# Kernel optimization log

Measured on AMD Instinct MI355X. Metric: run time of the kernel, lower is better.

The kernel has to match this reference:

```python
import jax, jax.numpy as jnp
import numpy as np

BS, V, N, C_IN, C_OUT = 8, 4096, 16, 64, 64


def setup_inputs() -> dict:
    key = jax.random.key(0)
    k1, k2, k3, k4, k5 = jax.random.split(key, 5)
    stdv = 1.0 / np.sqrt(N * C_IN)
    return {
        "neighbor_index": jax.random.randint(k1, (BS, V, N), 0, V, dtype=jnp.int64),
        "vertices": jax.random.normal(k2, (BS, V, 3), dtype=jnp.float32),
        "feature_map": jax.random.normal(k3, (BS, V, C_IN), dtype=jnp.float32),
        "weights": jax.random.uniform(k4, (C_OUT, (N + 1) * C_IN), dtype=jnp.float32, minval=-stdv, maxval=stdv),
        "bias": jax.random.uniform(k5, (C_OUT,), dtype=jnp.float32, minval=-stdv, maxval=stdv),
    }


def reference(neighbor_index, vertices, feature_map, weights, bias):
    bs, v, n = neighbor_index.shape
    # gather neighbor features per batch element: (bs, v, n, c)
    neighbors = jax.vmap(lambda f, idx: f[idx])(feature_map, neighbor_index)
    # prepend self feature: (bs, v, n+1, c)
    feats = jnp.concatenate([feature_map[:, :, None, :], neighbors], axis=2)
    # torch permutes to (bs, c, n+1, v) then reshapes -> flat index = c*(n+1)+k,
    # equivalent to transposing last two dims here before flattening
    flat = feats.transpose(0, 1, 3, 2).reshape(bs, v, -1)  # (bs, v, c*(n+1))
    out = jnp.einsum('bvf,of->bvo', flat, weights) + bias
    return jax.nn.relu(out)
```

## Files before the change

kernel.cpp:

```cpp
#include <hip/hip_runtime.h>
#include <stdint.h>

#define NV 4096

typedef __attribute__((ext_vector_type(8))) short bf16x8;
typedef __attribute__((ext_vector_type(4))) float f32x4;

__device__ __forceinline__ unsigned short f2bf(float f) {
  union { float f; unsigned int u; } v; v.f = f;
  unsigned int r = v.u + 0x7FFF + ((v.u >> 16) & 1);
  return (unsigned short)(r >> 16);
}

__global__ __launch_bounds__(256)
void prep(const float* __restrict__ fm, const float* __restrict__ w,
          unsigned short* __restrict__ fmb, unsigned short* __restrict__ wb) {
  int blk = blockIdx.x;
  if (blk < 1024) {
    int i = (blk * 256 + threadIdx.x) * 8;
    float4 v0 = *(const float4*)(fm + i);
    float4 v1 = *(const float4*)(fm + i + 4);
    ushort4 o0, o1;
    o0.x = f2bf(v0.x); o0.y = f2bf(v0.y); o0.z = f2bf(v0.z); o0.w = f2bf(v0.w);
    o1.x = f2bf(v1.x); o1.y = f2bf(v1.y); o1.z = f2bf(v1.z); o1.w = f2bf(v1.w);
    *(ushort4*)(fmb + i) = o0;
    *(ushort4*)(fmb + i + 4) = o1;
  } else {
    int t = (blk - 1024) * 256 + threadIdx.x;
    int c = t & 63;
    int o = (t >> 6) & 63;
    int k = t >> 12;
    wb[t] = f2bf(w[o * 1088 + c * 17 + k]);
  }
}

__global__ __launch_bounds__(512, 2)
void conv_main(const int* __restrict__ nbr, const unsigned short* __restrict__ fmb,
               const unsigned short* __restrict__ wb, const float* __restrict__ bias,
               float* __restrict__ out) {
  __shared__ unsigned short smem[17 * 4096];

  const int bid = blockIdx.x;
  const int b = bid & 7;
  const int tile = bid >> 3;
  const int tid = threadIdx.x;
  const int lane = tid & 63;
  const int lm = lane & 15;
  const int lk = lane >> 4;
  const int w8 = tid >> 6;
  const int rg = w8 >> 1;
  const int h = w8 & 1;

  const int rbase = tile * 128 + rg * 32;
  const int row0 = rbase + lm;
  const int row1 = rbase + 16 + lm;

  const bf16x8* fb = (const bf16x8*)(fmb + (size_t)b * NV * 64);

  const int4* n0 = (const int4*)(nbr + ((size_t)b * NV + row0) * 16) + h * 2;
  const int4* n1 = (const int4*)(nbr + ((size_t)b * NV + row1) * 16) + h * 2;
  const int4 i0a = n0[0], i0b = n0[1];
  const int4 i1a = n1[0], i1b = n1[1];

  const int off0 = lm * 128 + ((lk ^ (lm & 7)) << 4);
  const int off1 = off0 ^ 64;

  f32x4 acc00{0,0,0,0}, acc01{0,0,0,0}, acc02{0,0,0,0}, acc03{0,0,0,0};
  f32x4 acc10{0,0,0,0}, acc11{0,0,0,0}, acc12{0,0,0,0}, acc13{0,0,0,0};

  bf16x8 A0h0X, A0h1X, A1h0X, A1h1X;
  bf16x8 A0h0Y, A0h1Y, A1h0Y, A1h1Y;
  bf16x8 A0h0Z, A0h1Z, A1h0Z, A1h1Z;
  bf16x8 B0h0P, B1h0P, B2h0P, B3h0P, B0h1P, B1h1P, B2h1P, B3h1P;
  bf16x8 B0h0Q, B1h0Q, B2h0Q, B3h0Q, B0h1Q, B1h1Q, B2h1Q, B3h1Q;

#define SBR __builtin_amdgcn_sched_barrier(0)
#define MFMA __builtin_amdgcn_mfma_f32_16x16x32_bf16

#define LOADA(S, SV0, SV1) {                         \
    const bf16x8* p0_ = fb + (size_t)(SV0) * 8;      \
    const bf16x8* p1_ = fb + (size_t)(SV1) * 8;      \
    A0h0##S = p0_[lk];     A0h1##S = p0_[lk + 4];    \
    A1h0##S = p1_[lk];     A1h1##S = p1_[lk + 4];    \
  }

#define LOADB(S, KG) {                                          \
    const char* bp_ = ((const char*)smem) + (KG) * 8192;        \
    B0h0##S = *(const bf16x8*)(bp_ + 0 * 2048 + off0);          \
    B1h0##S = *(const bf16x8*)(bp_ + 1 * 2048 + off0);          \
    B2h0##S = *(const bf16x8*)(bp_ + 2 * 2048 + off0);          \
    B3h0##S = *(const bf16x8*)(bp_ + 3 * 2048 + off0);          \
    B0h1##S = *(const bf16x8*)(bp_ + 0 * 2048 + off1);          \
    B1h1##S = *(const bf16x8*)(bp_ + 1 * 2048 + off1);          \
    B2h1##S = *(const bf16x8*)(bp_ + 2 * 2048 + off1);          \
    B3h1##S = *(const bf16x8*)(bp_ + 3 * 2048 + off1);          \
  }

#define MM(SA, SB) {                                       \
    acc00 = MFMA(A0h0##SA, B0h0##SB, acc00, 0, 0, 0);      \
    acc01 = MFMA(A0h0##SA, B1h0##SB, acc01, 0, 0, 0);      \
    acc02 = MFMA(A0h0##SA, B2h0##SB, acc02, 0, 0, 0);      \
    acc03 = MFMA(A0h0##SA, B3h0##SB, acc03, 0, 0, 0);      \
    acc10 = MFMA(A1h0##SA, B0h0##SB, acc10, 0, 0, 0);      \
    acc11 = MFMA(A1h0##SA, B1h0##SB, acc11, 0, 0, 0);      \
    acc12 = MFMA(A1h0##SA, B2h0##SB, acc12, 0, 0, 0);      \
    acc13 = MFMA(A1h0##SA, B3h0##SB, acc13, 0, 0, 0);      \
    acc00 = MFMA(A0h1##SA, B0h1##SB, acc00, 0, 0, 0);      \
    acc01 = MFMA(A0h1##SA, B1h1##SB, acc01, 0, 0, 0);      \
    acc02 = MFMA(A0h1##SA, B2h1##SB, acc02, 0, 0, 0);      \
    acc03 = MFMA(A0h1##SA, B3h1##SB, acc03, 0, 0, 0);      \
    acc10 = MFMA(A1h1##SA, B0h1##SB, acc10, 0, 0, 0);      \
    acc11 = MFMA(A1h1##SA, B1h1##SB, acc11, 0, 0, 0);      \
    acc12 = MFMA(A1h1##SA, B2h1##SB, acc12, 0, 0, 0);      \
    acc13 = MFMA(A1h1##SA, B3h1##SB, acc13, 0, 0, 0);      \
  }

  const int sv00 = h ? i0a.x : row0;   const int sv10 = h ? i1a.x : row1;
  const int sv01 = h ? i0a.y : i0a.x;  const int sv11 = h ? i1a.y : i1a.x;
  const int sv02 = h ? i0a.z : i0a.y;  const int sv12 = h ? i1a.z : i1a.y;

  LOADA(X, sv00, sv10);
  LOADA(Y, sv01, sv11);

  #pragma unroll
  for (int i = 0; i < 17; ++i) {
    int t = i * 512 + tid;
    int slot = t >> 9;
    int r = (t >> 3) & 63;
    int sl = t & 7;
    int seg = sl ^ (r & 7);
    const unsigned short* src = wb + (size_t)slot * 4096 + r * 64 + seg * 8;
    unsigned short* dst = smem + (size_t)t * 8;
    __builtin_amdgcn_global_load_lds(
        (const __attribute__((address_space(1))) void*)src,
        (__attribute__((address_space(3))) void*)dst, 16, 0, 0);
  }
  __syncthreads();

  LOADA(Z, sv02, sv12);
  if (h == 0) { LOADB(P, 0); } else { LOADB(P, 9); }

  if (h == 0) {
    LOADB(Q, 1); SBR; MM(X, P); SBR; LOADA(X, i0a.z, i1a.z); SBR;
    LOADB(P, 2); SBR; MM(Y, Q); SBR; LOADA(Y, i0a.w, i1a.w); SBR;
    LOADB(Q, 3); SBR; MM(Z, P); SBR; LOADA(Z, i0b.x, i1b.x); SBR;
    LOADB(P, 4); SBR; MM(X, Q); SBR; LOADA(X, i0b.y, i1b.y); SBR;
    LOADB(Q, 5); SBR; MM(Y, P); SBR; LOADA(Y, i0b.z, i1b.z); SBR;
    LOADB(P, 6); SBR; MM(Z, Q); SBR; LOADA(Z, i0b.w, i1b.w); SBR;
    LOADB(Q, 7); SBR; MM(X, P); SBR;
    LOADB(P, 8); SBR; MM(Y, Q); SBR;
    MM(Z, P);
  } else {
    LOADB(Q, 10); SBR; MM(X, P); SBR; LOADA(X, i0a.w, i1a.w); SBR;
    LOADB(P, 11); SBR; MM(Y, Q); SBR; LOADA(Y, i0b.x, i1b.x); SBR;
    LOADB(Q, 12); SBR; MM(Z, P); SBR; LOADA(Z, i0b.y, i1b.y); SBR;
    LOADB(P, 13); SBR; MM(X, Q); SBR; LOADA(X, i0b.z, i1b.z); SBR;
    LOADB(Q, 14); SBR; MM(Y, P); SBR; LOADA(Y, i0b.w, i1b.w); SBR;
    LOADB(P, 15); SBR; MM(Z, Q); SBR;
    LOADB(Q, 16); SBR; MM(X, P); SBR;
    MM(Y, Q);
  }

#undef MM
#undef LOADB
#undef LOADA
#undef MFMA
#undef SBR

  __syncthreads();
  if (h == 1) {
    float* rp = (float*)smem + rg * 2048 + lane * 4;
    *(f32x4*)(rp + 0 * 256) = acc00;
    *(f32x4*)(rp + 1 * 256) = acc01;
    *(f32x4*)(rp + 2 * 256) = acc02;
    *(f32x4*)(rp + 3 * 256) = acc03;
    *(f32x4*)(rp + 4 * 256) = acc10;
    *(f32x4*)(rp + 5 * 256) = acc11;
    *(f32x4*)(rp + 6 * 256) = acc12;
    *(f32x4*)(rp + 7 * 256) = acc13;
  }
  __syncthreads();
  if (h == 0) {
    const float* rp = (const float*)smem + rg * 2048 + lane * 4;
    acc00 += *(const f32x4*)(rp + 0 * 256);
    acc01 += *(const f32x4*)(rp + 1 * 256);
    acc02 += *(const f32x4*)(rp + 2 * 256);
    acc03 += *(const f32x4*)(rp + 3 * 256);
    acc10 += *(const f32x4*)(rp + 4 * 256);
    acc11 += *(const f32x4*)(rp + 5 * 256);
    acc12 += *(const f32x4*)(rp + 6 * 256);
    acc13 += *(const f32x4*)(rp + 7 * 256);

    const float bv0 = bias[lm];
    const float bv1 = bias[16 + lm];
    const float bv2 = bias[32 + lm];
    const float bv3 = bias[48 + lm];
    float* op = out + (size_t)b * NV * 64;
    #pragma unroll
    for (int m = 0; m < 2; ++m) {
      const int gv = rbase + m * 16 + lk * 4;
      #pragma unroll
      for (int r = 0; r < 4; ++r) {
        float* orow = op + (size_t)(gv + r) * 64;
        if (m == 0) {
          orow[lm]      = fmaxf(acc00[r] + bv0, 0.f);
          orow[16 + lm] = fmaxf(acc01[r] + bv1, 0.f);
          orow[32 + lm] = fmaxf(acc02[r] + bv2, 0.f);
          orow[48 + lm] = fmaxf(acc03[r] + bv3, 0.f);
        } else {
          orow[lm]      = fmaxf(acc10[r] + bv0, 0.f);
          orow[16 + lm] = fmaxf(acc11[r] + bv1, 0.f);
          orow[32 + lm] = fmaxf(acc12[r] + bv2, 0.f);
          orow[48 + lm] = fmaxf(acc13[r] + bv3, 0.f);
        }
      }
    }
  }
}

extern "C" void kernel_launch(void* const* d_in, const int* in_sizes, int n_in,
                              void* d_out, int out_size, void* d_ws, size_t ws_size,
                              hipStream_t stream) {
  const int* nbr = (const int*)d_in[0];
  const float* fm = (const float*)d_in[2];
  const float* w = (const float*)d_in[3];
  const float* bias = (const float*)d_in[4];
  float* out = (float*)d_out;

  unsigned short* fmb = (unsigned short*)d_ws;
  unsigned short* wb = fmb + (size_t)8 * NV * 64;

  prep<<<1296, 256, 0, stream>>>(fm, w, fmb, wb);
  conv_main<<<256, 512, 0, stream>>>(nbr, fmb, wb, bias, out);
}
```

Baseline: 22.99 us.

## Issue all neighbor gathers upfront, swap MFMA operands for vectorized output stores

All 9 (or 8) neighbor feature rows per wave are gathered into registers before the weight LDS wait, using a manual vmcnt wait and s_barrier in place of the rolling double-buffered A/B schedule. MFMA operands are swapped (weights as A, features as B), so each lane's accumulator holds four consecutive output channels. This lets the epilogue write float4 stores and load bias as vectors. The aim is more memory-level parallelism for the gathers and fewer scalar global stores, at the cost of much higher VGPR pressure and reliance on a hand-tuned vmcnt count.

```diff
diff --git a/kernel.cpp b/kernel.cpp
--- a/kernel.cpp
+++ b/kernel.cpp
@@ -57,70 +57,10 @@
 
   const bf16x8* fb = (const bf16x8*)(fmb + (size_t)b * NV * 64);
 
-  const int4* n0 = (const int4*)(nbr + ((size_t)b * NV + row0) * 16) + h * 2;
-  const int4* n1 = (const int4*)(nbr + ((size_t)b * NV + row1) * 16) + h * 2;
-  const int4 i0a = n0[0], i0b = n0[1];
-  const int4 i1a = n1[0], i1b = n1[1];
-
-  const int off0 = lm * 128 + ((lk ^ (lm & 7)) << 4);
-  const int off1 = off0 ^ 64;
-
-  f32x4 acc00{0,0,0,0}, acc01{0,0,0,0}, acc02{0,0,0,0}, acc03{0,0,0,0};
-  f32x4 acc10{0,0,0,0}, acc11{0,0,0,0}, acc12{0,0,0,0}, acc13{0,0,0,0};
-
-  bf16x8 A0h0X, A0h1X, A1h0X, A1h1X;
-  bf16x8 A0h0Y, A0h1Y, A1h0Y, A1h1Y;
-  bf16x8 A0h0Z, A0h1Z, A1h0Z, A1h1Z;
-  bf16x8 B0h0P, B1h0P, B2h0P, B3h0P, B0h1P, B1h1P, B2h1P, B3h1P;
-  bf16x8 B0h0Q, B1h0Q, B2h0Q, B3h0Q, B0h1Q, B1h1Q, B2h1Q, B3h1Q;
-
-#define SBR __builtin_amdgcn_sched_barrier(0)
-#define MFMA __builtin_amdgcn_mfma_f32_16x16x32_bf16
-
-#define LOADA(S, SV0, SV1) {                         \
-    const bf16x8* p0_ = fb + (size_t)(SV0) * 8;      \
-    const bf16x8* p1_ = fb + (size_t)(SV1) * 8;      \
-    A0h0##S = p0_[lk];     A0h1##S = p0_[lk + 4];    \
-    A1h0##S = p1_[lk];     A1h1##S = p1_[lk + 4];    \
-  }
-
-#define LOADB(S, KG) {                                          \
-    const char* bp_ = ((const char*)smem) + (KG) * 8192;        \
-    B0h0##S = *(const bf16x8*)(bp_ + 0 * 2048 + off0);          \
-    B1h0##S = *(const bf16x8*)(bp_ + 1 * 2048 + off0);          \
-    B2h0##S = *(const bf16x8*)(bp_ + 2 * 2048 + off0);          \
-    B3h0##S = *(const bf16x8*)(bp_ + 3 * 2048 + off0);          \
-    B0h1##S = *(const bf16x8*)(bp_ + 0 * 2048 + off1);          \
-    B1h1##S = *(const bf16x8*)(bp_ + 1 * 2048 + off1);          \
-    B2h1##S = *(const bf16x8*)(bp_ + 2 * 2048 + off1);          \
-    B3h1##S = *(const bf16x8*)(bp_ + 3 * 2048 + off1);          \
-  }
-
-#define MM(SA, SB) {                                       \
-    acc00 = MFMA(A0h0##SA, B0h0##SB, acc00, 0, 0, 0);      \
-    acc01 = MFMA(A0h0##SA, B1h0##SB, acc01, 0, 0, 0);      \
-    acc02 = MFMA(A0h0##SA, B2h0##SB, acc02, 0, 0, 0);      \
-    acc03 = MFMA(A0h0##SA, B3h0##SB, acc03, 0, 0, 0);      \
-    acc10 = MFMA(A1h0##SA, B0h0##SB, acc10, 0, 0, 0);      \
-    acc11 = MFMA(A1h0##SA, B1h0##SB, acc11, 0, 0, 0);      \
-    acc12 = MFMA(A1h0##SA, B2h0##SB, acc12, 0, 0, 0);      \
-    acc13 = MFMA(A1h0##SA, B3h0##SB, acc13, 0, 0, 0);      \
-    acc00 = MFMA(A0h1##SA, B0h1##SB, acc00, 0, 0, 0);      \
-    acc01 = MFMA(A0h1##SA, B1h1##SB, acc01, 0, 0, 0);      \
-    acc02 = MFMA(A0h1##SA, B2h1##SB, acc02, 0, 0, 0);      \
-    acc03 = MFMA(A0h1##SA, B3h1##SB, acc03, 0, 0, 0);      \
-    acc10 = MFMA(A1h1##SA, B0h1##SB, acc10, 0, 0, 0);      \
-    acc11 = MFMA(A1h1##SA, B1h1##SB, acc11, 0, 0, 0);      \
-    acc12 = MFMA(A1h1##SA, B2h1##SB, acc12, 0, 0, 0);      \
-    acc13 = MFMA(A1h1##SA, B3h1##SB, acc13, 0, 0, 0);      \
-  }
-
-  const int sv00 = h ? i0a.x : row0;   const int sv10 = h ? i1a.x : row1;
-  const int sv01 = h ? i0a.y : i0a.x;  const int sv11 = h ? i1a.y : i1a.x;
-  const int sv02 = h ? i0a.z : i0a.y;  const int sv12 = h ? i1a.z : i1a.y;
-
-  LOADA(X, sv00, sv10);
-  LOADA(Y, sv01, sv11);
+  const int4* q0 = (const int4*)(nbr + ((size_t)b * NV + row0) * 16) + h * 2;
+  const int4* q1 = (const int4*)(nbr + ((size_t)b * NV + row1) * 16) + h * 2;
+  const int4 i0a = q0[0], i0b = q0[1];
+  const int4 i1a = q1[0], i1b = q1[1];
 
   #pragma unroll
   for (int i = 0; i < 17; ++i) {
@@ -135,37 +75,91 @@
         (const __attribute__((address_space(1))) void*)src,
         (__attribute__((address_space(3))) void*)dst, 16, 0, 0);
   }
-  __syncthreads();
-
-  LOADA(Z, sv02, sv12);
-  if (h == 0) { LOADB(P, 0); } else { LOADB(P, 9); }
+  __builtin_amdgcn_sched_barrier(0);
+
+  bf16x8 F0m0h0, F0m0h1, F0m1h0, F0m1h1;
+  bf16x8 F1m0h0, F1m0h1, F1m1h0, F1m1h1;
+  bf16x8 F2m0h0, F2m0h1, F2m1h0, F2m1h1;
+  bf16x8 F3m0h0, F3m0h1, F3m1h0, F3m1h1;
+  bf16x8 F4m0h0, F4m0h1, F4m1h0, F4m1h1;
+  bf16x8 F5m0h0, F5m0h1, F5m1h0, F5m1h1;
+  bf16x8 F6m0h0, F6m0h1, F6m1h0, F6m1h1;
+  bf16x8 F7m0h0, F7m0h1, F7m1h0, F7m1h1;
+  bf16x8 F8m0h0, F8m0h1, F8m1h0, F8m1h1;
+
+#define LOADF(J, SV0, SV1) {                          \
+    const bf16x8* p0_ = fb + (size_t)(SV0) * 8;       \
+    const bf16x8* p1_ = fb + (size_t)(SV1) * 8;       \
+    F##J##m0h0 = p0_[lk];  F##J##m0h1 = p0_[lk + 4];  \
+    F##J##m1h0 = p1_[lk];  F##J##m1h1 = p1_[lk + 4];  \
+  }
 
   if (h == 0) {
-    LOADB(Q, 1); SBR; MM(X, P); SBR; LOADA(X, i0a.z, i1a.z); SBR;
-    LOADB(P, 2); SBR; MM(Y, Q); SBR; LOADA(Y, i0a.w, i1a.w); SBR;
-    LOADB(Q, 3); SBR; MM(Z, P); SBR; LOADA(Z, i0b.x, i1b.x); SBR;
-    LOADB(P, 4); SBR; MM(X, Q); SBR; LOADA(X, i0b.y, i1b.y); SBR;
-    LOADB(Q, 5); SBR; MM(Y, P); SBR; LOADA(Y, i0b.z, i1b.z); SBR;
-    LOADB(P, 6); SBR; MM(Z, Q); SBR; LOADA(Z, i0b.w, i1b.w); SBR;
-    LOADB(Q, 7); SBR; MM(X, P); SBR;
-    LOADB(P, 8); SBR; MM(Y, Q); SBR;
-    MM(Z, P);
+    LOADF(0, row0, row1);
+    LOADF(1, i0a.x, i1a.x); LOADF(2, i0a.y, i1a.y);
+    LOADF(3, i0a.z, i1a.z); LOADF(4, i0a.w, i1a.w);
+    LOADF(5, i0b.x, i1b.x); LOADF(6, i0b.y, i1b.y);
+    LOADF(7, i0b.z, i1b.z); LOADF(8, i0b.w, i1b.w);
   } else {
-    LOADB(Q, 10); SBR; MM(X, P); SBR; LOADA(X, i0a.w, i1a.w); SBR;
-    LOADB(P, 11); SBR; MM(Y, Q); SBR; LOADA(Y, i0b.x, i1b.x); SBR;
-    LOADB(Q, 12); SBR; MM(Z, P); SBR; LOADA(Z, i0b.y, i1b.y); SBR;
-    LOADB(P, 13); SBR; MM(X, Q); SBR; LOADA(X, i0b.z, i1b.z); SBR;
-    LOADB(Q, 14); SBR; MM(Y, P); SBR; LOADA(Y, i0b.w, i1b.w); SBR;
-    LOADB(P, 15); SBR; MM(Z, Q); SBR;
-    LOADB(Q, 16); SBR; MM(X, P); SBR;
-    MM(Y, Q);
-  }
-
-#undef MM
-#undef LOADB
-#undef LOADA
+    LOADF(0, i0a.x, i1a.x); LOADF(1, i0a.y, i1a.y);
+    LOADF(2, i0a.z, i1a.z); LOADF(3, i0a.w, i1a.w);
+    LOADF(4, i0b.x, i1b.x); LOADF(5, i0b.y, i1b.y);
+    LOADF(6, i0b.z, i1b.z); LOADF(7, i0b.w, i1b.w);
+  }
+
+  __builtin_amdgcn_sched_barrier(0);
+  if (h == 0) { asm volatile("s_waitcnt vmcnt(36)" ::: "memory"); }
+  else        { asm volatile("s_waitcnt vmcnt(32)" ::: "memory"); }
+  __builtin_amdgcn_sched_barrier(0);
+  __builtin_amdgcn_s_barrier();
+  __builtin_amdgcn_sched_barrier(0);
+
+  const int off0 = lm * 128 + ((lk ^ (lm & 7)) << 4);
+  const int off1 = off0 ^ 64;
+
+  f32x4 acc00{0,0,0,0}, acc01{0,0,0,0}, acc02{0,0,0,0}, acc03{0,0,0,0};
+  f32x4 acc10{0,0,0,0}, acc11{0,0,0,0}, acc12{0,0,0,0}, acc13{0,0,0,0};
+
+#define MFMA __builtin_amdgcn_mfma_f32_16x16x32_bf16
+#define PHASE(J, SLOT) {                                            \
+    const char* bp_ = ((const char*)smem) + (SLOT) * 8192;          \
+    bf16x8 W0a = *(const bf16x8*)(bp_ + 0 * 2048 + off0);           \
+    bf16x8 W0b = *(const bf16x8*)(bp_ + 0 * 2048 + off1);           \
+    bf16x8 W1a = *(const bf16x8*)(bp_ + 1 * 2048 + off0);           \
+    bf16x8 W1b = *(const bf16x8*)(bp_ + 1 * 2048 + off1);           \
+    bf16x8 W2a = *(const bf16x8*)(bp_ + 2 * 2048 + off0);           \
+    bf16x8 W2b = *(const bf16x8*)(bp_ + 2 * 2048 + off1);           \
+    bf16x8 W3a = *(const bf16x8*)(bp_ + 3 * 2048 + off0);           \
+    bf16x8 W3b = *(const bf16x8*)(bp_ + 3 * 2048 + off1);           \
+    acc00 = MFMA(W0a, F##J##m0h0, acc00, 0, 0, 0);                  \
+    acc00 = MFMA(W0b, F##J##m0h1, acc00, 0, 0, 0);                  \
+    acc10 = MFMA(W0a, F##J##m1h0, acc10, 0, 0, 0);                  \
+    acc10 = MFMA(W0b, F##J##m1h1, acc10, 0, 0, 0);                  \
+    acc01 = MFMA(W1a, F##J##m0h0, acc01, 0, 0, 0);                  \
+    acc01 = MFMA(W1b, F##J##m0h1, acc01, 0, 0, 0);                  \
+    acc11 = MFMA(W1a, F##J##m1h0, acc11, 0, 0, 0);                  \
+    acc11 = MFMA(W1b, F##J##m1h1, acc11, 0, 0, 0);                  \
+    acc02 = MFMA(W2a, F##J##m0h0, acc02, 0, 0, 0);                  \
+    acc02 = MFMA(W2b, F##J##m0h1, acc02, 0, 0, 0);                  \
+    acc12 = MFMA(W2a, F##J##m1h0, acc12, 0, 0, 0);                  \
+    acc12 = MFMA(W2b, F##J##m1h1, acc12, 0, 0, 0);                  \
+    acc03 = MFMA(W3a, F##J##m0h0, acc03, 0, 0, 0);                  \
+    acc03 = MFMA(W3b, F##J##m0h1, acc03, 0, 0, 0);                  \
+    acc13 = MFMA(W3a, F##J##m1h0, acc13, 0, 0, 0);                  \
+    acc13 = MFMA(W3b, F##J##m1h1, acc13, 0, 0, 0);                  \
+  }
+
+  if (h == 0) {
+    PHASE(0, 0); PHASE(1, 1); PHASE(2, 2); PHASE(3, 3); PHASE(4, 4);
+    PHASE(5, 5); PHASE(6, 6); PHASE(7, 7); PHASE(8, 8);
+  } else {
+    PHASE(0, 9); PHASE(1, 10); PHASE(2, 11); PHASE(3, 12);
+    PHASE(4, 13); PHASE(5, 14); PHASE(6, 15); PHASE(7, 16);
+  }
+
+#undef PHASE
 #undef MFMA
-#undef SBR
+#undef LOADF
 
   __syncthreads();
   if (h == 1) {
@@ -191,30 +185,25 @@
     acc12 += *(const f32x4*)(rp + 6 * 256);
     acc13 += *(const f32x4*)(rp + 7 * 256);
 
-    const float bv0 = bias[lm];
-    const float bv1 = bias[16 + lm];
-    const float bv2 = bias[32 + lm];
-    const float bv3 = bias[48 + lm];
+    const f32x4 bv0 = *(const f32x4*)(bias + 0  + lk * 4);
+    const f32x4 bv1 = *(const f32x4*)(bias + 16 + lk * 4);
+    const f32x4 bv2 = *(const f32x4*)(bias + 32 + lk * 4);
+    const f32x4 bv3 = *(const f32x4*)(bias + 48 + lk * 4);
     float* op = out + (size_t)b * NV * 64;
-    #pragma unroll
-    for (int m = 0; m < 2; ++m) {
-      const int gv = rbase + m * 16 + lk * 4;
-      #pragma unroll
-      for (int r = 0; r < 4; ++r) {
-        float* orow = op + (size_t)(gv + r) * 64;
-        if (m == 0) {
-          orow[lm]      = fmaxf(acc00[r] + bv0, 0.f);
-          orow[16 + lm] = fmaxf(acc01[r] + bv1, 0.f);
-          orow[32 + lm] = fmaxf(acc02[r] + bv2, 0.f);
-          orow[48 + lm] = fmaxf(acc03[r] + bv3, 0.f);
-        } else {
-          orow[lm]      = fmaxf(acc10[r] + bv0, 0.f);
-          orow[16 + lm] = fmaxf(acc11[r] + bv1, 0.f);
-          orow[32 + lm] = fmaxf(acc12[r] + bv2, 0.f);
-          orow[48 + lm] = fmaxf(acc13[r] + bv3, 0.f);
-        }
-      }
-    }
+
+#define STORE1(ACC, BV, V, N) {                                   \
+    f32x4 t_ = ACC + BV;                                          \
+    t_[0] = fmaxf(t_[0], 0.f); t_[1] = fmaxf(t_[1], 0.f);         \
+    t_[2] = fmaxf(t_[2], 0.f); t_[3] = fmaxf(t_[3], 0.f);         \
+    *(f32x4*)(op + (size_t)(V) * 64 + (N) * 16 + lk * 4) = t_;    \
+  }
+    const int v0 = rbase + lm;
+    const int v1 = rbase + 16 + lm;
+    STORE1(acc00, bv0, v0, 0); STORE1(acc01, bv1, v0, 1);
+    STORE1(acc02, bv2, v0, 2); STORE1(acc03, bv3, v0, 3);
+    STORE1(acc10, bv0, v1, 0); STORE1(acc11, bv1, v1, 1);
+    STORE1(acc12, bv2, v1, 2); STORE1(acc13, bv3, v1, 3);
+#undef STORE1
   }
 }
 
```

Result: slower. 25.01 us (+8.8%).
